# Optimization experiments

Measured on AMD Instinct MI355X. Metric: run time of the kernel, lower is better.

Reference implementation:

```python
import jax, jax.numpy as jnp
import numpy as np

EPS = 1e-8
CUTOFF = 7.0
B, A, EPG = 128, 100, 2048
N, E = B * A, B * EPG
LAT, HID, FCH, NRBF, NTYPES, NT = 256, 128, 512, 16, 100, 50


def _lattice(lengths, angles):
    # pymatgen-style lattice_params_to_matrix; angles in degrees. -> [B,3,3] rows are a,b,c vectors
    a, b, c = lengths[:, 0], lengths[:, 1], lengths[:, 2]
    al, be, ga = (jnp.radians(angles[:, k]) for k in range(3))
    val = (jnp.cos(al) * jnp.cos(be) - jnp.cos(ga)) / (jnp.sin(al) * jnp.sin(be))
    gs = jnp.arccos(jnp.clip(val, -1.0, 1.0))
    z = jnp.zeros_like(a)
    va = jnp.stack([a * jnp.sin(be), z, a * jnp.cos(be)], -1)
    vb = jnp.stack([-b * jnp.sin(al) * jnp.cos(gs), b * jnp.sin(al) * jnp.sin(gs), b * jnp.cos(al)], -1)
    vc = jnp.stack([z, z, c], -1)
    return jnp.stack([va, vb, vc], 1)


def setup_inputs() -> dict:
    rng = np.random.default_rng(0)
    # sorted-per-graph edge list with i != j (so no_iden_mask is all-true)
    i = rng.integers(0, A, (B, EPG))
    j = (i + rng.integers(1, A, (B, EPG))) % A
    order = np.argsort(i * A + j, axis=1, kind='stable')
    i = np.take_along_axis(i, order, 1)
    j = np.take_along_axis(j, order, 1)
    goff = (np.arange(B) * A)[:, None]
    edge_index = np.stack([(j + goff).reshape(-1), (i + goff).reshape(-1)]).astype(np.int32)  # [2,E], row0=j(src), row1=i(dst)
    to_jimages = rng.integers(-1, 2, (E, 3)).astype(np.int32)
    batch = np.repeat(np.arange(B), A).astype(np.int32)
    num_atoms = np.full((B,), A, np.int32)
    atom_types = rng.integers(0, NTYPES, (N,)).astype(np.int32)
    time_steps = rng.integers(0, NT, (B,)).astype(np.int32)

    ks = jax.random.split(jax.random.key(0), 12)
    f32 = jnp.float32
    inp = dict(
        latents=jax.random.normal(ks[0], (B, LAT), f32),
        gt_frac_coords=jax.random.uniform(ks[1], (N, 3), f32),
        lengths=8.0 + 4.0 * jax.random.uniform(ks[2], (B, 3), f32),
        angles=90.0 + 8.0 * (jax.random.uniform(ks[3], (B, 3), f32) - 0.5),
        coord_noise=jax.random.normal(ks[4], (N, 3), f32),
        sigmas=jnp.exp(jnp.linspace(np.log(0.01), np.log(10.0), NT)).astype(f32),
        atom_emb=jax.random.normal(ks[5], (NTYPES, HID), f32),
        rbf_W=0.05 * jax.random.normal(ks[6], (NRBF, HID), f32),
        rbf_b=jnp.zeros((HID,), f32),
        bb_W=0.1 * jax.random.normal(ks[7], (HID, HID), f32),
        bb_b=jnp.zeros((HID,), f32),
        sc_W0=0.05 * jax.random.normal(ks[8], (LAT + HID, FCH), f32),
        sc_b0=jnp.zeros((FCH,), f32),
        sc_W1=0.05 * jax.random.normal(ks[9], (FCH, FCH), f32),
        sc_b1=jnp.zeros((FCH,), f32),
        sc_W2=0.05 * jax.random.normal(ks[10], (FCH, 1), f32),
        sc_b2=jnp.zeros((1,), f32),
        num_atoms=jnp.asarray(num_atoms),
        atom_types=jnp.asarray(atom_types),
        batch=jnp.asarray(batch),
        edge_index=jnp.asarray(edge_index),
        to_jimages=jnp.asarray(to_jimages),
        time_steps=jnp.asarray(time_steps),
    )
    return inp


def reference(latents, gt_frac_coords, lengths, angles, coord_noise, sigmas,
              atom_emb, rbf_W, rbf_b, bb_W, bb_b,
              sc_W0, sc_b0, sc_W1, sc_b1, sc_W2, sc_b2,
              num_atoms, atom_types, batch, edge_index, to_jimages, time_steps):
    seg_sum = jax.ops.segment_sum
    L = _lattice(lengths, angles)            # [B,3,3]
    Linv = jnp.linalg.inv(L)
    Ln, Lni = L[batch], Linv[batch]          # per-node lattice [N,3,3]
    cart_gt = jnp.einsum('ni,nij->nj', gt_frac_coords, Ln)
    sig_node = sigmas[time_steps][batch][:, None]              # [N,1]
    pert = cart_gt + sig_node * coord_noise
    # correct_cart_coords: wrap back into unit cell
    frac_p = jnp.einsum('ni,nij->nj', pert, Lni) % 1.0
    pert = jnp.einsum('ni,nij->nj', frac_p, Ln)
    jn, iN = edge_index[0], edge_index[1]
    offs = jnp.einsum('ei,eij->ej', to_jimages.astype(pert.dtype), L[batch[jn]])
    dvec = pert[iN] - pert[jn] - offs                           # [E,3]
    dist = jnp.linalg.norm(dvec, axis=-1)
    # backbone: atom-type embeddings + Gaussian RBF edge MLP -> [E,HID]
    mus = jnp.linspace(0.0, CUTOFF, rbf_W.shape[0]).astype(pert.dtype)
    rbf = jnp.exp(-10.0 * (dist[:, None] - mus) ** 2)
    h = atom_emb[atom_types]
    ef = jax.nn.silu((h[jn] + h[iN] + rbf @ rbf_W + rbf_b) @ bb_W + bb_b)
    # latents repeat_interleave(num_multi_edge_per_graph) == gather by edge's graph id
    ef = jnp.concatenate([ef, latents[batch[jn]]], axis=1)      # [E, HID+LAT]
    hh = jax.nn.relu(ef @ sc_W0 + sc_b0)
    hh = jax.nn.relu(hh @ sc_W1 + sc_b1)
    scores = hh @ sc_W2 + sc_b2                                 # [E,1]
    # align_gt_cart_coords: minimum-image gt coords relative to perturbed coords
    frac_gt = jnp.einsum('ni,nij->nj', cart_gt, Lni)
    fd = frac_gt - frac_p
    fd = fd - jnp.round(fd)
    aligned = pert + jnp.einsum('ni,nij->nj', fd, Ln)
    gt_dvec = aligned[iN] - aligned[jn] - offs
    gt_d = jnp.linalg.norm(gt_dvec, axis=-1, keepdims=True)
    pd = dist[:, None]
    gt_scores = gt_d - pd
    # per_node loss: group multi-edges by contiguous (i,j) runs
    start = jnp.concatenate([jnp.ones((1,), bool), (iN[1:] != iN[:-1]) | (jn[1:] != jn[:-1])])
    seg = jnp.cumsum(start.astype(jnp.int32)) - 1               # [E], < E segments
    cnt = seg_sum(jnp.ones((E,), pert.dtype), seg, num_segments=E)
    c = jnp.maximum(cnt, 1.0)
    sv = scores * dvec / (pd + EPS)
    gv = gt_scores * dvec / (pd + EPS)
    sE = seg_sum(sv, seg, num_segments=E) / c[:, None]
    gE = seg_sum(gv, seg, num_segments=E) / c[:, None]
    recv = jnp.round(seg_sum(iN.astype(pert.dtype), seg, num_segments=E) / c).astype(jnp.int32)
    sN = seg_sum(sE, recv, num_segments=N)                      # scores_per_node_pos [N,3]
    gN = seg_sum(gE, recv, num_segments=N)
    sq = (sN - gN / sig_node) ** 2
    na = num_atoms.astype(pert.dtype)[:, None]
    score_loss = (seg_sum(sq, batch, num_segments=B) / na).mean()
    # pbc symmetry regularizer
    preds = pert + sN / sig_node
    center = seg_sum(preds, batch, num_segments=B) / na
    dc = preds - center[batch]
    pbs = (jnp.abs(dc[:, 0].max() + dc[:, 0].min())
           + jnp.abs(dc[:, 1].max() + dc[:, 1].min())
           + jnp.abs(dc[:, 2].max() + dc[:, 2].min()))
    return (score_loss, pbs)
```

## Files before the change

kernel.cpp:

```cpp
#include <hip/hip_runtime.h>
#include <hip/hip_bf16.h>

namespace {
constexpr int Bb = 128, Nn = 12800, Ee = 262144;
constexpr int LAT = 256, HID = 128, FCH = 512, NRBF = 16;
constexpr int TE = 64;
constexpr int TSTRIDE = 1040;
constexpr int RBF_OFF = 16640;

constexpr int WS_L      = 0;
constexpr int WS_LI     = 1152;
constexpr int WS_SIG    = 2304;
constexpr int WS_RBFW2  = 2432;
constexpr int WS_CVEC   = 4480;
constexpr int WS_HB     = 4608;
constexpr int WS_LATP   = 17408;
constexpr int WS_PERT   = 82944;
constexpr int WS_ALIGN  = 121344;
constexpr int WS_SN     = 159744;
constexpr int WS_GN     = 198144;
constexpr int WS_PREDS  = 236544;
constexpr int WS_BSUM   = 274944;
constexpr int WS_CENTER = 275328;
constexpr int WS_MINMAX = 275712;
constexpr int WS_W0T_F   = 276000;
constexpr int WS_W1T_F   = 308768;
constexpr int WS_RBFW2T_F = 439840;
}

typedef short bf16x8 __attribute__((ext_vector_type(8)));
typedef unsigned short u16x8 __attribute__((ext_vector_type(8)));
typedef float f32x4 __attribute__((ext_vector_type(4)));

static __device__ __forceinline__ unsigned short f2bf(float f) {
  unsigned int u = __float_as_uint(f);
  unsigned int r = (u + 0x7fffu + ((u >> 16) & 1u)) >> 16;
  return (unsigned short)r;
}
static __device__ __forceinline__ unsigned int pk2bf(float a, float b) {
  unsigned int r;
  asm("v_cvt_pk_bf16_f32 %0, %1, %2" : "=v"(r) : "v"(a), "v"(b));
  return r;
}
static __device__ __forceinline__ float fastrcp(float x) {
  return __builtin_amdgcn_rcpf(x);
}

static __device__ __forceinline__ void make_lattice(
    const float* lengths, const float* angles, int b, float L[9], float Li[9]) {
  float a = lengths[b * 3 + 0], bl = lengths[b * 3 + 1], c = lengths[b * 3 + 2];
  const float d2r = 0.017453292519943295f;
  float al = angles[b * 3 + 0] * d2r, be = angles[b * 3 + 1] * d2r, ga = angles[b * 3 + 2] * d2r;
  float ca = cosf(al), cb = cosf(be), cg = cosf(ga), sa = sinf(al), sb = sinf(be);
  float val = (ca * cb - cg) / (sa * sb);
  val = fminf(1.f, fmaxf(-1.f, val));
  float gs = acosf(val);
  L[0] = a * sb;              L[1] = 0.f;                L[2] = a * cb;
  L[3] = -bl * sa * cosf(gs); L[4] = bl * sa * sinf(gs); L[5] = bl * ca;
  L[6] = 0.f;                 L[7] = 0.f;                L[8] = c;
  float det = L[0] * (L[4] * L[8] - L[5] * L[7])
            - L[1] * (L[3] * L[8] - L[5] * L[6])
            + L[2] * (L[3] * L[7] - L[4] * L[6]);
  float id = 1.f / det;
  Li[0] =  (L[4] * L[8] - L[5] * L[7]) * id;
  Li[1] = -(L[1] * L[8] - L[2] * L[7]) * id;
  Li[2] =  (L[1] * L[5] - L[2] * L[4]) * id;
  Li[3] = -(L[3] * L[8] - L[5] * L[6]) * id;
  Li[4] =  (L[0] * L[8] - L[2] * L[6]) * id;
  Li[5] = -(L[0] * L[5] - L[2] * L[3]) * id;
  Li[6] =  (L[3] * L[7] - L[4] * L[6]) * id;
  Li[7] = -(L[0] * L[7] - L[1] * L[6]) * id;
  Li[8] =  (L[0] * L[4] - L[1] * L[3]) * id;
}

static __device__ __forceinline__ void atomicMaxFloat(float* addr, float val) {
  int* ai = reinterpret_cast<int*>(addr);
  int old = *ai;
  while (__int_as_float(old) < val) {
    int assumed = old;
    old = atomicCAS(ai, assumed, __float_as_int(val));
    if (old == assumed) break;
  }
}
static __device__ __forceinline__ void atomicMinFloat(float* addr, float val) {
  int* ai = reinterpret_cast<int*>(addr);
  int old = *ai;
  while (__int_as_float(old) > val) {
    int assumed = old;
    old = atomicCAS(ai, assumed, __float_as_int(val));
    if (old == assumed) break;
  }
}

__global__ __launch_bounds__(256) void k_pre(
    const float* lengths, const float* angles, const float* sigmas, const int* tsteps,
    const float* aemb, const float* bbW, const float* rbfW, const float* rbfb,
    const float* bbb, const float* latents, const float* scW0, const float* scb0,
    const float* scW1, const float* gtf, const float* noise, const int* batch,
    const int* atype, unsigned short* w0t, unsigned short* w1t,
    unsigned short* rbfw2t, float* ws) {
  const int blk = blockIdx.x, t = threadIdx.x;
  if (blk < 304) {
    int gid = blk * 256 + t;
    if (gid < 2 * Nn * 3) ws[WS_SN + gid] = 0.f;
    else if (gid < 2 * Nn * 3 + 2 * Bb * 3) ws[WS_BSUM + (gid - 2 * Nn * 3)] = 0.f;
    else if (gid < 2 * Nn * 3 + 2 * Bb * 3 + 3) ws[WS_MINMAX + (gid - 2 * Nn * 3 - 2 * Bb * 3)] = -3.0e38f;
    else if (gid < 2 * Nn * 3 + 2 * Bb * 3 + 6) ws[WS_MINMAX + (gid - 2 * Nn * 3 - 2 * Bb * 3)] = 3.0e38f;
  } else if (blk == 304) {
    int b = t;
    if (b >= Bb) return;
    float L[9], Li[9];
    make_lattice(lengths, angles, b, L, Li);
#pragma unroll
    for (int i = 0; i < 9; ++i) {
      ws[WS_L + b * 9 + i] = L[i];
      ws[WS_LI + b * 9 + i] = Li[i];
    }
    ws[WS_SIG + b] = sigmas[tsteps[b]];
  } else if (blk < 405) {
    int tile = blk - 305;
    if (t < HID) {
      float acc = 0.f;
      for (int k = 0; k < HID; ++k) acc += aemb[tile * HID + k] * bbW[k * HID + t];
      ws[WS_HB + tile * HID + t] = acc;
    }
  } else if (blk == 405) {
    if (t < HID) {
      float accs[NRBF];
#pragma unroll
      for (int k = 0; k < NRBF; ++k) accs[k] = 0.f;
      float accb = 0.f;
      for (int m = 0; m < HID; ++m) {
        float w = bbW[m * HID + t];
#pragma unroll
        for (int k = 0; k < NRBF; ++k) accs[k] += rbfW[k * HID + m] * w;
        accb += rbfb[m] * w;
      }
#pragma unroll
      for (int k = 0; k < NRBF; ++k) ws[WS_RBFW2 + k * HID + t] = accs[k];
      ws[WS_CVEC + t] = accb + bbb[t];
    }
  } else if (blk < 534) {
    int b = blk - 406;
    __shared__ float lat[LAT];
    lat[t] = latents[b * LAT + t];
    __syncthreads();
    int c0 = 2 * t;
    float a0 = 0.f, a1 = 0.f;
    for (int m = 0; m < LAT; ++m) {
      float2 w = *reinterpret_cast<const float2*>(scW0 + (HID + m) * FCH + c0);
      float lm = lat[m];
      a0 += lm * w.x;
      a1 += lm * w.y;
    }
    ws[WS_LATP + b * FCH + c0] = a0 + scb0[c0];
    ws[WS_LATP + b * FCH + c0 + 1] = a1 + scb0[c0 + 1];
  } else if (blk < 566) {
    int id8 = (blk - 534) * 256 + t;
    int tile = id8 >> 6, lf = id8 & 63;
    int colTile = tile >> 2, kTile = tile & 3;
    int col = colTile * 16 + (lf & 15);
    int kbase = kTile * 32 + (lf >> 4) * 8;
    u16x8 v;
#pragma unroll
    for (int e = 0; e < 8; ++e) v[e] = f2bf(scW0[(kbase + e) * FCH + col]);
    *(u16x8*)(w0t + id8 * 8) = v;
  } else if (blk < 694) {
    int id8 = (blk - 566) * 256 + t;
    int tile = id8 >> 6, lf = id8 & 63;
    int colTile = tile >> 4, kTile = tile & 15;
    int col = colTile * 16 + (lf & 15);
    int kbase = kTile * 32 + (lf >> 4) * 8;
    u16x8 v;
#pragma unroll
    for (int e = 0; e < 8; ++e) v[e] = f2bf(scW1[(kbase + e) * FCH + col]);
    *(u16x8*)(w1t + id8 * 8) = v;
  } else if (blk < 696) {
    int id = (blk - 694) * 256 + t;
    if (id < 512) {
      int tile = id >> 6, lf = id & 63;
      int c = tile * 16 + (lf & 15);
      u16x8 v;
#pragma unroll
      for (int e = 0; e < 8; ++e) {
        int k = (lf >> 4) * 8 + e;
        if (k < NRBF) {
          float acc = 0.f;
          for (int m = 0; m < HID; ++m) acc += rbfW[k * HID + m] * bbW[m * HID + c];
          v[e] = f2bf(acc);
        } else {
          v[e] = 0;
        }
      }
      *(u16x8*)(rbfw2t + id * 8) = v;
    }
  } else {
    int n = (blk - 696) * 256 + t;
    if (n >= Nn) return;
    int b = batch[n];
    float L[9], Li[9];
    make_lattice(lengths, angles, b, L, Li);
    float sig = sigmas[tsteps[b]];
    float f0 = gtf[n * 3], f1 = gtf[n * 3 + 1], f2 = gtf[n * 3 + 2];
    float cg[3], p0[3], fp[3], pe[3], fg[3], fd[3];
#pragma unroll
    for (int j = 0; j < 3; ++j) cg[j] = f0 * L[j] + f1 * L[3 + j] + f2 * L[6 + j];
#pragma unroll
    for (int j = 0; j < 3; ++j) p0[j] = cg[j] + sig * noise[n * 3 + j];
#pragma unroll
    for (int j = 0; j < 3; ++j) {
      float v = p0[0] * Li[j] + p0[1] * Li[3 + j] + p0[2] * Li[6 + j];
      fp[j] = v - floorf(v);
    }
#pragma unroll
    for (int j = 0; j < 3; ++j) pe[j] = fp[0] * L[j] + fp[1] * L[3 + j] + fp[2] * L[6 + j];
#pragma unroll
    for (int j = 0; j < 3; ++j) fg[j] = cg[0] * Li[j] + cg[1] * Li[3 + j] + cg[2] * Li[6 + j];
#pragma unroll
    for (int j = 0; j < 3; ++j) { float d = fg[j] - fp[j]; fd[j] = d - rintf(d); }
#pragma unroll
    for (int j = 0; j < 3; ++j) {
      ws[WS_PERT + n * 3 + j] = pe[j];
      ws[WS_ALIGN + n * 3 + j] = pe[j] + fd[0] * L[j] + fd[1] * L[3 + j] + fd[2] * L[6 + j];
    }
  }
}

__global__ __launch_bounds__(512, 4) void k_edge(
    const int* ei, const int* toj, const int* batch, const int* atype,
    const unsigned short* w0t, const unsigned short* w1t,
    const unsigned short* rbfw2t,
    const float* scb1, const float* scW2, const float* scb2, float* ws) {
  __shared__ __align__(16) char s_hh_b[64 * TSTRIDE];
  __shared__ float s_dvec[TE][3];
  __shared__ float s_dist[TE], s_gtd[TE];
  __shared__ int s_tj[TE], s_ti[TE];
  __shared__ float s_wsum[8][TE];

  char* s_ef_b = s_hh_b;

  const int t = threadIdx.x;
  const int e0 = blockIdx.x * TE;
  const int b0 = batch[ei[e0]];

  const int lane = t & 63;
  const int wv = t >> 6;
  const int el = lane & 15;
  const int q  = lane >> 4;

  if (t < TE) {
    int e = e0 + t;
    int jn = ei[e], iN = ei[Ee + e];
    int b = batch[jn];
    float tx = (float)toj[e * 3], ty = (float)toj[e * 3 + 1], tz = (float)toj[e * 3 + 2];
    const float* L = ws + WS_L + b * 9;
    float dv[3], gv[3];
#pragma unroll
    for (int j = 0; j < 3; ++j) {
      float off = tx * L[j] + ty * L[3 + j] + tz * L[6 + j];
      dv[j] = ws[WS_PERT + iN * 3 + j] - ws[WS_PERT + jn * 3 + j] - off;
      gv[j] = ws[WS_ALIGN + iN * 3 + j] - ws[WS_ALIGN + jn * 3 + j] - off;
    }
    float dist = sqrtf(dv[0] * dv[0] + dv[1] * dv[1] + dv[2] * dv[2]);
    float gtd = sqrtf(gv[0] * gv[0] + gv[1] * gv[1] + gv[2] * gv[2]);
#pragma unroll
    for (int j = 0; j < 3; ++j) s_dvec[t][j] = dv[j];
    s_dist[t] = dist;
    s_gtd[t] = gtd;
    s_tj[t] = atype[jn]; s_ti[t] = atype[iN];
    const float step = 7.0f / 15.0f;
    int el0 = t & 15, q0 = t >> 4;
#pragma unroll
    for (int n = 0; n < 4; ++n) {
      float dn = __shfl(dist, n * 16 + el0);
      unsigned int wb0 = 0, wb1 = 0, wb2 = 0, wb3 = 0;
      if (q0 < 2) {
        float d0 = dn - (float)(8 * q0) * step;
#pragma unroll
        for (int p = 0; p < 4; ++p) {
          float m0 = d0 - (float)(2 * p) * step;
          float m1 = m0 - step;
          unsigned int r = pk2bf(__expf(-10.f * m0 * m0), __expf(-10.f * m1 * m1));
          if (p == 0) wb0 = r; else if (p == 1) wb1 = r;
          else if (p == 2) wb2 = r; else wb3 = r;
        }
      }
      uint4 u = {wb0, wb1, wb2, wb3};
      *(uint4*)(s_hh_b + RBF_OFF + n * 1024 + t * 16) = u;
    }
  }
  __syncthreads();

  {
    bf16x8 arb = *(const bf16x8*)(rbfw2t + wv * 512 + lane * 8);
    bf16x8 brb[4];
#pragma unroll
    for (int n = 0; n < 4; ++n)
      brb[n] = *(const bf16x8*)(s_hh_b + RBF_OFF + n * 1024 + lane * 16);
    f32x4 accB[4];
#pragma unroll
    for (int n = 0; n < 4; ++n)
      accB[n] = __builtin_amdgcn_mfma_f32_16x16x32_bf16(
          arb, brb[n], (f32x4){0.f, 0.f, 0.f, 0.f}, 0, 0, 0);
    int col0 = wv * 16 + q * 4;
    float4 cv = *(const float4*)(ws + WS_CVEC + col0);
    int kT = wv >> 1;
    int oct = (wv & 1) * 2 + (q >> 1);
#pragma unroll
    for (int n = 0; n < 4; ++n) {
      int eg = n * 16 + el;
      int tj = s_tj[eg], ti = s_ti[eg];
      float4 hj = *(const float4*)(ws + WS_HB + tj * HID + col0);
      float4 hi = *(const float4*)(ws + WS_HB + ti * HID + col0);
      f32x4 a = accB[n];
      float z0 = a[0] + hj.x + hi.x + cv.x;
      float z1 = a[1] + hj.y + hi.y + cv.y;
      float z2 = a[2] + hj.z + hi.z + cv.z;
      float z3 = a[3] + hj.w + hi.w + cv.w;
      float s0 = z0 * fastrcp(1.f + __expf(-z0));
      float s1 = z1 * fastrcp(1.f + __expf(-z1));
      float s2 = z2 * fastrcp(1.f + __expf(-z2));
      float s3 = z3 * fastrcp(1.f + __expf(-z3));
      uint2 val = {pk2bf(s0, s1), pk2bf(s2, s3)};
      int addr = (kT * 4 + n) * TSTRIDE + (el + 16 * oct) * 16 + (q & 1) * 8;
      *(uint2*)(s_ef_b + addr) = val;
    }
  }
  __syncthreads();

  {
    f32x4 acc[4][4];
#pragma unroll
    for (int m = 0; m < 4; ++m)
#pragma unroll
      for (int n = 0; n < 4; ++n) acc[m][n] = (f32x4){0.f, 0.f, 0.f, 0.f};
    const unsigned short* w0base = w0t + (size_t)(wv * 4) * 4 * 512 + lane * 8;
#pragma unroll
    for (int kt = 0; kt < 4; ++kt) {
      bf16x8 aw[4];
#pragma unroll
      for (int m = 0; m < 4; ++m)
        aw[m] = *(const bf16x8*)(w0base + (size_t)(m * 4 + kt) * 512);
      bf16x8 bf[4];
#pragma unroll
      for (int n = 0; n < 4; ++n)
        bf[n] = *(const bf16x8*)(s_ef_b + (kt * 4 + n) * TSTRIDE + lane * 16);
      __builtin_amdgcn_s_setprio(1);
#pragma unroll
      for (int n = 0; n < 4; ++n)
#pragma unroll
        for (int m = 0; m < 4; ++m)
          acc[m][n] = __builtin_amdgcn_mfma_f32_16x16x32_bf16(aw[m], bf[n], acc[m][n], 0, 0, 0);
      __builtin_amdgcn_s_setprio(0);
    }
    __syncthreads();
#pragma unroll
    for (int m = 0; m < 4; ++m) {
      float4 lp = *(const float4*)(ws + WS_LATP + b0 * FCH + wv * 64 + m * 16 + q * 4);
#pragma unroll
      for (int n = 0; n < 4; ++n) {
        f32x4 v = acc[m][n];
        float h0 = fmaxf(v[0] + lp.x, 0.f);
        float h1 = fmaxf(v[1] + lp.y, 0.f);
        float h2 = fmaxf(v[2] + lp.z, 0.f);
        float h3 = fmaxf(v[3] + lp.w, 0.f);
        uint2 val = {pk2bf(h0, h1), pk2bf(h2, h3)};
        int kT = wv * 2 + (m >> 1);
        int oct = (m & 1) * 2 + (q >> 1);
        int addr = (kT * 4 + n) * TSTRIDE + (el + 16 * oct) * 16 + (q & 1) * 8;
        *(uint2*)(s_hh_b + addr) = val;
      }
    }
  }
  __syncthreads();

  {
    f32x4 acc[4][4];
#pragma unroll
    for (int m = 0; m < 4; ++m)
#pragma unroll
      for (int n = 0; n < 4; ++n) acc[m][n] = (f32x4){0.f, 0.f, 0.f, 0.f};
    const unsigned short* w1base = w1t + (size_t)(wv * 4) * 16 * 512 + lane * 8;
#pragma unroll 4
    for (int kt = 0; kt < 16; ++kt) {
      bf16x8 aw[4];
#pragma unroll
      for (int m = 0; m < 4; ++m)
        aw[m] = *(const bf16x8*)(w1base + (size_t)(m * 16 + kt) * 512);
      bf16x8 bf[4];
#pragma unroll
      for (int n = 0; n < 4; ++n)
        bf[n] = *(const bf16x8*)(s_hh_b + (kt * 4 + n) * TSTRIDE + lane * 16);
      __builtin_amdgcn_s_setprio(1);
#pragma unroll
      for (int n = 0; n < 4; ++n)
#pragma unroll
        for (int m = 0; m < 4; ++m)
          acc[m][n] = __builtin_amdgcn_mfma_f32_16x16x32_bf16(aw[m], bf[n], acc[m][n], 0, 0, 0);
      __builtin_amdgcn_s_setprio(0);
    }
    float p[4] = {0.f, 0.f, 0.f, 0.f};
#pragma unroll
    for (int m = 0; m < 4; ++m) {
      int colb = wv * 64 + m * 16 + q * 4;
      float4 b1v = *(const float4*)(scb1 + colb);
      float4 w2v = *(const float4*)(scW2 + colb);
#pragma unroll
      for (int n = 0; n < 4; ++n) {
        f32x4 v = acc[m][n];
        p[n] += fmaxf(v[0] + b1v.x, 0.f) * w2v.x;
        p[n] += fmaxf(v[1] + b1v.y, 0.f) * w2v.y;
        p[n] += fmaxf(v[2] + b1v.z, 0.f) * w2v.z;
        p[n] += fmaxf(v[3] + b1v.w, 0.f) * w2v.w;
      }
    }
#pragma unroll
    for (int n = 0; n < 4; ++n) {
      float x = p[n];
      x += __shfl_xor(x, 16);
      x += __shfl_xor(x, 32);
      p[n] = x;
    }
    if (lane < 16) {
#pragma unroll
      for (int n = 0; n < 4; ++n) s_wsum[wv][n * 16 + el] = p[n];
    }
  }
  __syncthreads();

  if (t < TE) {
    int e = e0 + t;
    float score = scb2[0];
#pragma unroll
    for (int w = 0; w < 8; ++w) score += s_wsum[w][t];
    int jn = ei[e], iN = ei[Ee + e];
    int s = e;
    while (s > 0 && ei[s - 1] == jn && ei[Ee + s - 1] == iN) --s;
    int en = e;
    while (en + 1 < Ee && ei[en + 1] == jn && ei[Ee + en + 1] == iN) ++en;
    float invc = fastrcp((float)(en - s + 1));
    float dist = s_dist[t];
    float rden = fastrcp(dist + 1e-8f);
    float gts = s_gtd[t] - dist;
#pragma unroll
    for (int j = 0; j < 3; ++j) {
      float dir = s_dvec[t][j] * rden;
      atomicAdd(&ws[WS_SN + iN * 3 + j], score * dir * invc);
      atomicAdd(&ws[WS_GN + iN * 3 + j], gts * dir * invc);
    }
  }
}

__global__ void k_node2(const int* batch, float* ws) {
  int n = blockIdx.x * blockDim.x + threadIdx.x;
  int lane = threadIdx.x & 63;
  int b = batch[n];
  float sig = ws[WS_SIG + b];
  float v[6];
#pragma unroll
  for (int j = 0; j < 3; ++j) {
    float s = ws[WS_SN + n * 3 + j], g = ws[WS_GN + n * 3 + j];
    float d = s - g / sig;
    v[j] = d * d;
    float pr = ws[WS_PERT + n * 3 + j] + s / sig;
    ws[WS_PREDS + n * 3 + j] = pr;
    v[3 + j] = pr;
  }
  int g0 = __shfl(b, 0);
  bool in0 = (b == g0);
  unsigned long long m1 = __ballot(!in0);
#pragma unroll
  for (int seg = 0; seg < 2; ++seg) {
    int gs, leader;
    bool inseg;
    if (seg == 0) {
      gs = g0; leader = 0; inseg = in0;
    } else {
      if (m1 == 0ULL) break;
      leader = __ffsll(m1) - 1;
      gs = __shfl(b, leader);
      inseg = !in0;
    }
    float sv[6];
#pragma unroll
    for (int k = 0; k < 6; ++k) {
      float x = inseg ? v[k] : 0.f;
      x += __shfl_xor(x, 1);
      x += __shfl_xor(x, 2);
      x += __shfl_xor(x, 4);
      x += __shfl_xor(x, 8);
      x += __shfl_xor(x, 16);
      x += __shfl_xor(x, 32);
      sv[k] = x;
    }
    if (lane == leader) {
#pragma unroll
      for (int j = 0; j < 3; ++j) {
        atomicAdd(&ws[WS_BSUM + gs * 3 + j], sv[j]);
        atomicAdd(&ws[WS_CENTER + gs * 3 + j], sv[3 + j]);
      }
    }
  }
}

__global__ void k_minmax(const int* batch, const int* num_atoms, float* ws) {
  int n = blockIdx.x * blockDim.x + threadIdx.x;
  int lane = threadIdx.x & 63, wid = threadIdx.x >> 6;
  float mx[3], mn[3];
  if (n < Nn) {
    int b = batch[n];
    float na = (float)num_atoms[b];
#pragma unroll
    for (int j = 0; j < 3; ++j) {
      float v = ws[WS_PREDS + n * 3 + j] - ws[WS_CENTER + b * 3 + j] / na;
      mx[j] = v; mn[j] = v;
    }
  } else {
#pragma unroll
    for (int j = 0; j < 3; ++j) { mx[j] = -3.0e38f; mn[j] = 3.0e38f; }
  }
#pragma unroll
  for (int off = 32; off >= 1; off >>= 1) {
#pragma unroll
    for (int j = 0; j < 3; ++j) {
      mx[j] = fmaxf(mx[j], __shfl_xor(mx[j], off));
      mn[j] = fminf(mn[j], __shfl_xor(mn[j], off));
    }
  }
  __shared__ float smx[4][3], smn[4][3];
  if (lane == 0) {
#pragma unroll
    for (int j = 0; j < 3; ++j) { smx[wid][j] = mx[j]; smn[wid][j] = mn[j]; }
  }
  __syncthreads();
  if (threadIdx.x == 0) {
#pragma unroll
    for (int j = 0; j < 3; ++j) {
      float M = fmaxf(fmaxf(smx[0][j], smx[1][j]), fmaxf(smx[2][j], smx[3][j]));
      float m = fminf(fminf(smn[0][j], smn[1][j]), fminf(smn[2][j], smn[3][j]));
      atomicMaxFloat(&ws[WS_MINMAX + j], M);
      atomicMinFloat(&ws[WS_MINMAX + 3 + j], m);
    }
  }
}

__global__ void k_final(const int* num_atoms, const float* ws, float* out) {
  int t = threadIdx.x;
  float loss = 0.f;
  if (t < Bb) {
    float na = (float)num_atoms[t];
    loss = (ws[WS_BSUM + t * 3] + ws[WS_BSUM + t * 3 + 1] + ws[WS_BSUM + t * 3 + 2]) / na;
  }
#pragma unroll
  for (int off = 32; off >= 1; off >>= 1) loss += __shfl_xor(loss, off);
  __shared__ float s2[2];
  if ((t & 63) == 0) s2[t >> 6] = loss;
  __syncthreads();
  if (t == 0) {
    float L = (s2[0] + s2[1]) / (3.0f * (float)Bb);
    float pbs = fabsf(ws[WS_MINMAX + 0] + ws[WS_MINMAX + 3]) +
                fabsf(ws[WS_MINMAX + 1] + ws[WS_MINMAX + 4]) +
                fabsf(ws[WS_MINMAX + 2] + ws[WS_MINMAX + 5]);
    out[0] = L;
    out[1] = pbs;
  }
}

extern "C" void kernel_launch(void* const* d_in, const int* in_sizes, int n_in,
                              void* d_out, int out_size, void* d_ws, size_t ws_size,
                              hipStream_t stream) {
  const float* latents = (const float*)d_in[0];
  const float* gtf     = (const float*)d_in[1];
  const float* lengths = (const float*)d_in[2];
  const float* angles  = (const float*)d_in[3];
  const float* noise   = (const float*)d_in[4];
  const float* sigmas  = (const float*)d_in[5];
  const float* aemb    = (const float*)d_in[6];
  const float* rbfW    = (const float*)d_in[7];
  const float* rbfb    = (const float*)d_in[8];
  const float* bbW     = (const float*)d_in[9];
  const float* bbb     = (const float*)d_in[10];
  const float* scW0    = (const float*)d_in[11];
  const float* scb0    = (const float*)d_in[12];
  const float* scW1    = (const float*)d_in[13];
  const float* scb1    = (const float*)d_in[14];
  const float* scW2    = (const float*)d_in[15];
  const float* scb2    = (const float*)d_in[16];
  const int* num_atoms = (const int*)d_in[17];
  const int* atype     = (const int*)d_in[18];
  const int* batch     = (const int*)d_in[19];
  const int* ei        = (const int*)d_in[20];
  const int* toj       = (const int*)d_in[21];
  const int* tsteps    = (const int*)d_in[22];
  float* ws = (float*)d_ws;
  float* out = (float*)d_out;
  unsigned short* w0t = (unsigned short*)(ws + WS_W0T_F);
  unsigned short* w1t = (unsigned short*)(ws + WS_W1T_F);
  unsigned short* rbfw2t = (unsigned short*)(ws + WS_RBFW2T_F);

  hipLaunchKernelGGL(k_pre, dim3(746), dim3(256), 0, stream,
                     lengths, angles, sigmas, tsteps, aemb, bbW, rbfW, rbfb, bbb,
                     latents, scW0, scb0, scW1, gtf, noise, batch, atype,
                     w0t, w1t, rbfw2t, ws);
  hipLaunchKernelGGL(k_edge, dim3(Ee / TE), dim3(512), 0, stream,
                     ei, toj, batch, atype, w0t, w1t, rbfw2t, scb1, scW2, scb2, ws);
  hipLaunchKernelGGL(k_node2, dim3(50), dim3(256), 0, stream, batch, ws);
  hipLaunchKernelGGL(k_minmax, dim3(50), dim3(256), 0, stream, batch, num_atoms, ws);
  hipLaunchKernelGGL(k_final, dim3(1), dim3(128), 0, stream, num_atoms, ws, out);
}
```

Baseline: 268.0 us.

## Switch edge MLP GEMMs from 16x16x32 to 32x32x16 bf16 MFMA tiles

Both edge-MLP GEMM stages now use 32x32x16 bf16 MFMA instructions with 2x2 accumulator tiles per wave instead of 4x4 tiles of 16x16x32. The pre-swizzled weight layouts for W0 and W1 and the LDS activation read/write addressing are rebuilt to match the 32-lane fragment format, and the final reduction needs one fewer cross-lane shuffle. The intent is fewer MFMA issues, fewer fragment loads per FLOP and more operand reuse. The larger instruction has longer latency, and the new LDS access pattern may bring bank conflicts.

```diff
diff --git a/kernel.cpp b/kernel.cpp
--- a/kernel.cpp
+++ b/kernel.cpp
@@ -31,6 +31,7 @@
 typedef short bf16x8 __attribute__((ext_vector_type(8)));
 typedef unsigned short u16x8 __attribute__((ext_vector_type(8)));
 typedef float f32x4 __attribute__((ext_vector_type(4)));
+typedef float f32x16 __attribute__((ext_vector_type(16)));
 
 static __device__ __forceinline__ unsigned short f2bf(float f) {
   unsigned int u = __float_as_uint(f);
@@ -157,20 +158,20 @@
     ws[WS_LATP + b * FCH + c0 + 1] = a1 + scb0[c0 + 1];
   } else if (blk < 566) {
     int id8 = (blk - 534) * 256 + t;
-    int tile = id8 >> 6, lf = id8 & 63;
-    int colTile = tile >> 2, kTile = tile & 3;
-    int col = colTile * 16 + (lf & 15);
-    int kbase = kTile * 32 + (lf >> 4) * 8;
+    int f = id8 >> 6, lf = id8 & 63;
+    int P = f >> 3, h = f & 7;
+    int col = P * 32 + (lf & 31);
+    int kbase = h * 16 + (lf >> 5) * 8;
     u16x8 v;
 #pragma unroll
     for (int e = 0; e < 8; ++e) v[e] = f2bf(scW0[(kbase + e) * FCH + col]);
     *(u16x8*)(w0t + id8 * 8) = v;
   } else if (blk < 694) {
     int id8 = (blk - 566) * 256 + t;
-    int tile = id8 >> 6, lf = id8 & 63;
-    int colTile = tile >> 4, kTile = tile & 15;
-    int col = colTile * 16 + (lf & 15);
-    int kbase = kTile * 32 + (lf >> 4) * 8;
+    int f = id8 >> 6, lf = id8 & 63;
+    int P = f >> 5, h = f & 31;
+    int col = P * 32 + (lf & 31);
+    int kbase = h * 16 + (lf >> 5) * 8;
     u16x8 v;
 #pragma unroll
     for (int e = 0; e < 8; ++e) v[e] = f2bf(scW1[(kbase + e) * FCH + col]);
@@ -247,6 +248,8 @@
   const int wv = t >> 6;
   const int el = lane & 15;
   const int q  = lane >> 4;
+  const int e16 = (lane & 31) >> 4;
+  const int hi5 = lane >> 5;
 
   if (t < TE) {
     int e = e0 + t;
@@ -329,101 +332,110 @@
   __syncthreads();
 
   {
-    f32x4 acc[4][4];
-#pragma unroll
-    for (int m = 0; m < 4; ++m)
-#pragma unroll
-      for (int n = 0; n < 4; ++n) acc[m][n] = (f32x4){0.f, 0.f, 0.f, 0.f};
-    const unsigned short* w0base = w0t + (size_t)(wv * 4) * 4 * 512 + lane * 8;
-#pragma unroll
-    for (int kt = 0; kt < 4; ++kt) {
-      bf16x8 aw[4];
-#pragma unroll
-      for (int m = 0; m < 4; ++m)
-        aw[m] = *(const bf16x8*)(w0base + (size_t)(m * 4 + kt) * 512);
-      bf16x8 bf[4];
-#pragma unroll
-      for (int n = 0; n < 4; ++n)
-        bf[n] = *(const bf16x8*)(s_ef_b + (kt * 4 + n) * TSTRIDE + lane * 16);
+    f32x16 acc[2][2];
+#pragma unroll
+    for (int m = 0; m < 2; ++m)
+#pragma unroll
+      for (int n = 0; n < 2; ++n)
+#pragma unroll
+        for (int r = 0; r < 16; ++r) acc[m][n][r] = 0.f;
+    const unsigned short* w0b = w0t + (size_t)(wv * 2) * 8 * 512 + lane * 8;
+#pragma unroll
+    for (int h = 0; h < 8; ++h) {
+      bf16x8 aw[2];
+#pragma unroll
+      for (int m = 0; m < 2; ++m)
+        aw[m] = *(const bf16x8*)(w0b + (size_t)(m * 8 + h) * 512);
+      int kT = h >> 1;
+      int oct = (h & 1) * 2 + hi5;
+      bf16x8 bf[2];
+#pragma unroll
+      for (int n = 0; n < 2; ++n)
+        bf[n] = *(const bf16x8*)(s_ef_b + (kT * 4 + n * 2 + e16) * TSTRIDE + (el + 16 * oct) * 16);
       __builtin_amdgcn_s_setprio(1);
 #pragma unroll
-      for (int n = 0; n < 4; ++n)
-#pragma unroll
-        for (int m = 0; m < 4; ++m)
-          acc[m][n] = __builtin_amdgcn_mfma_f32_16x16x32_bf16(aw[m], bf[n], acc[m][n], 0, 0, 0);
+      for (int n = 0; n < 2; ++n)
+#pragma unroll
+        for (int m = 0; m < 2; ++m)
+          acc[m][n] = __builtin_amdgcn_mfma_f32_32x32x16_bf16(aw[m], bf[n], acc[m][n], 0, 0, 0);
       __builtin_amdgcn_s_setprio(0);
     }
     __syncthreads();
 #pragma unroll
-    for (int m = 0; m < 4; ++m) {
-      float4 lp = *(const float4*)(ws + WS_LATP + b0 * FCH + wv * 64 + m * 16 + q * 4);
-#pragma unroll
-      for (int n = 0; n < 4; ++n) {
-        f32x4 v = acc[m][n];
-        float h0 = fmaxf(v[0] + lp.x, 0.f);
-        float h1 = fmaxf(v[1] + lp.y, 0.f);
-        float h2 = fmaxf(v[2] + lp.z, 0.f);
-        float h3 = fmaxf(v[3] + lp.w, 0.f);
-        uint2 val = {pk2bf(h0, h1), pk2bf(h2, h3)};
-        int kT = wv * 2 + (m >> 1);
-        int oct = (m & 1) * 2 + (q >> 1);
-        int addr = (kT * 4 + n) * TSTRIDE + (el + 16 * oct) * 16 + (q & 1) * 8;
-        *(uint2*)(s_hh_b + addr) = val;
+    for (int m = 0; m < 2; ++m) {
+#pragma unroll
+      for (int g = 0; g < 4; ++g) {
+        float4 lp = *(const float4*)(ws + WS_LATP + b0 * FCH + wv * 64 + m * 32 + g * 8 + 4 * hi5);
+#pragma unroll
+        for (int n = 0; n < 2; ++n) {
+          float h0 = fmaxf(acc[m][n][4 * g + 0] + lp.x, 0.f);
+          float h1 = fmaxf(acc[m][n][4 * g + 1] + lp.y, 0.f);
+          float h2 = fmaxf(acc[m][n][4 * g + 2] + lp.z, 0.f);
+          float h3 = fmaxf(acc[m][n][4 * g + 3] + lp.w, 0.f);
+          uint2 val = {pk2bf(h0, h1), pk2bf(h2, h3)};
+          int addr = ((wv * 2 + m) * 4 + n * 2 + e16) * TSTRIDE + (el + 16 * g) * 16 + hi5 * 8;
+          *(uint2*)(s_hh_b + addr) = val;
+        }
       }
     }
   }
   __syncthreads();
 
   {
-    f32x4 acc[4][4];
-#pragma unroll
-    for (int m = 0; m < 4; ++m)
-#pragma unroll
-      for (int n = 0; n < 4; ++n) acc[m][n] = (f32x4){0.f, 0.f, 0.f, 0.f};
-    const unsigned short* w1base = w1t + (size_t)(wv * 4) * 16 * 512 + lane * 8;
-#pragma unroll 4
-    for (int kt = 0; kt < 16; ++kt) {
-      bf16x8 aw[4];
-#pragma unroll
-      for (int m = 0; m < 4; ++m)
-        aw[m] = *(const bf16x8*)(w1base + (size_t)(m * 16 + kt) * 512);
-      bf16x8 bf[4];
-#pragma unroll
-      for (int n = 0; n < 4; ++n)
-        bf[n] = *(const bf16x8*)(s_hh_b + (kt * 4 + n) * TSTRIDE + lane * 16);
+    f32x16 acc[2][2];
+#pragma unroll
+    for (int m = 0; m < 2; ++m)
+#pragma unroll
+      for (int n = 0; n < 2; ++n)
+#pragma unroll
+        for (int r = 0; r < 16; ++r) acc[m][n][r] = 0.f;
+    const unsigned short* w1b = w1t + (size_t)(wv * 2) * 32 * 512 + lane * 8;
+#pragma unroll 8
+    for (int h = 0; h < 32; ++h) {
+      bf16x8 aw[2];
+#pragma unroll
+      for (int m = 0; m < 2; ++m)
+        aw[m] = *(const bf16x8*)(w1b + (size_t)(m * 32 + h) * 512);
+      int kT = h >> 1;
+      int oct = (h & 1) * 2 + hi5;
+      bf16x8 bf[2];
+#pragma unroll
+      for (int n = 0; n < 2; ++n)
+        bf[n] = *(const bf16x8*)(s_hh_b + (kT * 4 + n * 2 + e16) * TSTRIDE + (el + 16 * oct) * 16);
       __builtin_amdgcn_s_setprio(1);
 #pragma unroll
-      for (int n = 0; n < 4; ++n)
-#pragma unroll
-        for (int m = 0; m < 4; ++m)
-          acc[m][n] = __builtin_amdgcn_mfma_f32_16x16x32_bf16(aw[m], bf[n], acc[m][n], 0, 0, 0);
+      for (int n = 0; n < 2; ++n)
+#pragma unroll
+        for (int m = 0; m < 2; ++m)
+          acc[m][n] = __builtin_amdgcn_mfma_f32_32x32x16_bf16(aw[m], bf[n], acc[m][n], 0, 0, 0);
       __builtin_amdgcn_s_setprio(0);
     }
-    float p[4] = {0.f, 0.f, 0.f, 0.f};
-#pragma unroll
-    for (int m = 0; m < 4; ++m) {
-      int colb = wv * 64 + m * 16 + q * 4;
-      float4 b1v = *(const float4*)(scb1 + colb);
-      float4 w2v = *(const float4*)(scW2 + colb);
-#pragma unroll
-      for (int n = 0; n < 4; ++n) {
-        f32x4 v = acc[m][n];
-        p[n] += fmaxf(v[0] + b1v.x, 0.f) * w2v.x;
-        p[n] += fmaxf(v[1] + b1v.y, 0.f) * w2v.y;
-        p[n] += fmaxf(v[2] + b1v.z, 0.f) * w2v.z;
-        p[n] += fmaxf(v[3] + b1v.w, 0.f) * w2v.w;
+    float p[2] = {0.f, 0.f};
+#pragma unroll
+    for (int m = 0; m < 2; ++m) {
+#pragma unroll
+      for (int g = 0; g < 4; ++g) {
+        int colb = wv * 64 + m * 32 + g * 8 + 4 * hi5;
+        float4 b1v = *(const float4*)(scb1 + colb);
+        float4 w2v = *(const float4*)(scW2 + colb);
+#pragma unroll
+        for (int n = 0; n < 2; ++n) {
+          p[n] += fmaxf(acc[m][n][4 * g + 0] + b1v.x, 0.f) * w2v.x;
+          p[n] += fmaxf(acc[m][n][4 * g + 1] + b1v.y, 0.f) * w2v.y;
+          p[n] += fmaxf(acc[m][n][4 * g + 2] + b1v.z, 0.f) * w2v.z;
+          p[n] += fmaxf(acc[m][n][4 * g + 3] + b1v.w, 0.f) * w2v.w;
+        }
       }
     }
 #pragma unroll
-    for (int n = 0; n < 4; ++n) {
+    for (int n = 0; n < 2; ++n) {
       float x = p[n];
-      x += __shfl_xor(x, 16);
       x += __shfl_xor(x, 32);
       p[n] = x;
     }
-    if (lane < 16) {
-#pragma unroll
-      for (int n = 0; n < 4; ++n) s_wsum[wv][n * 16 + el] = p[n];
+    if (lane < 32) {
+#pragma unroll
+      for (int n = 0; n < 2; ++n) s_wsum[wv][n * 32 + lane] = p[n];
     }
   }
   __syncthreads();
```

Result: slower. 298.0 us (+11.2%).
